# Kernel tuning notes

Hardware: AMD Instinct MI355X
Metric: run time of the kernel (lower is better)

Reference implementation:

```python
import jax, jax.numpy as jnp
import numpy as np

NOT_EPSILON = 1.0
B, K, Q, T = 2, 512, 512, 128


def swishmax(x, axis):
    # x * exp(x - max) normalized by sum(|.|) + 1 along `axis`
    xexp = x * jnp.exp(x - jnp.max(x, axis=axis, keepdims=True))
    return xexp / (jnp.sum(jnp.abs(xexp), axis=axis, keepdims=True) + NOT_EPSILON)


def setup_inputs() -> dict:
    key = jax.random.key(0)
    ks = jax.random.split(key, 8)
    scale = 1.0 / np.sqrt(T)
    return {
        "query_tokens": jax.random.normal(ks[0], (B, Q, T), dtype=jnp.float32),
        "key_tokens": jax.random.normal(ks[1], (B, K, T), dtype=jnp.float32),
        "value_tokens": jax.random.normal(ks[2], (B, K, T), dtype=jnp.float32),
        "Wk": jax.random.normal(ks[3], (T, T), dtype=jnp.float32) * scale,
        "Wq": jax.random.normal(ks[4], (T, T), dtype=jnp.float32) * scale,
        "Wv": jax.random.normal(ks[5], (T, T), dtype=jnp.float32) * scale,
        "Wl": jax.random.normal(ks[6], (T, T), dtype=jnp.float32) * scale,
        "Wo": jax.random.normal(ks[7], (T, T), dtype=jnp.float32) * scale,
    }


def reference(query_tokens, key_tokens, value_tokens, Wk, Wq, Wv, Wl, Wo):
    lin = lambda x, W: jnp.einsum('...t,ut->...u', x, W)  # nn.Linear(bias=False): x @ W.T
    k = lin(key_tokens, Wk)       # [B, K, T]
    q = lin(query_tokens, Wq)     # [B, Q, T]
    # outer-product broadcast over tokens: [B, K, Q, T]
    attention_raw = k[..., :, None, :] * q[..., None, :, :]
    attention_logits = lin(attention_raw, Wl)            # [B, K, Q, T]
    attention_scale = swishmax(attention_logits, axis=-2)  # normalize over Q (dim=-2)
    v = lin(value_tokens, Wv)     # [B, K, T]
    values_scaled = v[..., :, None, :] * attention_scale  # [B, K, Q, T]
    value_sum = values_scaled.sum(axis=-3)                # sum over K -> [B, Q, T]
    return lin(value_sum, Wo)
```

## Files before the change

### kernel.cpp

```cpp
#include <hip/hip_runtime.h>


using f16    = _Float16;
using f16x4  = __attribute__((ext_vector_type(4)))  f16;
using f16x8  = __attribute__((ext_vector_type(8)))  f16;
using f32x16 = __attribute__((ext_vector_type(16))) float;

#define LOG2E 1.4426950408889634f

__device__ __forceinline__ float exp2b(float x) {
  return __builtin_amdgcn_exp2f(x);
}

__device__ __forceinline__ f16x8 cvt8(float4 a, float4 b) {
  f16x8 r;
  r[0]=(f16)a.x; r[1]=(f16)a.y; r[2]=(f16)a.z; r[3]=(f16)a.w;
  r[4]=(f16)b.x; r[5]=(f16)b.y; r[6]=(f16)b.z; r[7]=(f16)b.w;
  return r;
}

__global__ __launch_bounds__(256, 2) void k1_proj(
    const float* __restrict__ q_tok, const float* __restrict__ k_tok,
    const float* __restrict__ v_tok, const float* __restrict__ Wq,
    const float* __restrict__ Wk,    const float* __restrict__ Wv,
    f16* __restrict__ qh, float* __restrict__ kls, float* __restrict__ vf)
{
  const int gid    = blockIdx.x;
  const int tensor = gid >> 4;
  const int sub    = gid & 15;
  const int b      = sub >> 3;
  const int rt     = sub & 7;
  const float* X = tensor==0 ? q_tok : (tensor==1 ? k_tok : v_tok);
  const float* W = tensor==0 ? Wq    : (tensor==1 ? Wk    : Wv);

  const int tid = threadIdx.x;
  const int w = tid >> 6, lane = tid & 63;
  const int l31 = lane & 31, lhi = lane >> 5;
  const int rbase = rt*64 + (w>>1)*32;
  const int cbase = (w&1)*64;

  f32x16 C0, C1;
  #pragma unroll
  for (int i=0;i<16;++i){ C0[i]=0.f; C1[i]=0.f; }

  #pragma unroll
  for (int kc=0; kc<8; ++kc) {
    const float* ap = X + (size_t)(b*512 + rbase + l31)*128 + kc*16 + 8*lhi;
    f16x8 a = cvt8(*(const float4*)ap, *(const float4*)(ap+4));
    const float* bp0 = W + (size_t)(cbase + l31)*128 + kc*16 + 8*lhi;
    f16x8 b0 = cvt8(*(const float4*)bp0, *(const float4*)(bp0+4));
    C0 = __builtin_amdgcn_mfma_f32_32x32x16_f16(a, b0, C0, 0, 0, 0);
    const float* bp1 = bp0 + 32*128;
    f16x8 b1 = cvt8(*(const float4*)bp1, *(const float4*)(bp1+4));
    C1 = __builtin_amdgcn_mfma_f32_32x32x16_f16(a, b1, C1, 0, 0, 0);
  }

  #pragma unroll
  for (int us=0; us<2; ++us) {
    #pragma unroll
    for (int r=0; r<16; ++r) {
      const int row = rbase + (r&3) + 8*(r>>2) + 4*lhi;
      const int col = cbase + us*32 + l31;
      const float val = us ? C1[r] : C0[r];
      const size_t idx = (size_t)(b*512 + row)*128 + col;
      if (tensor==0)      qh[idx]  = (f16)val;
      else if (tensor==1) kls[idx] = val * LOG2E;
      else                vf[idx]  = val;
    }
  }
}

__global__ __launch_bounds__(1024, 4) void k2_main(
    const f16* __restrict__ qh, const float* __restrict__ kls,
    const float* __restrict__ vf, const float* __restrict__ Wl,
    f16* __restrict__ part)
{
  const int gid  = blockIdx.x;
  const int b    = gid >> 7;
  const int uq   = (gid >> 5) & 3;
  const int grp  = gid & 31;
  const int kk0  = grp * 16;

  const int tid = threadIdx.x;
  const int w = tid >> 6, lane = tid & 63;
  const int l31 = lane & 31, lhi = lane >> 5;
  const int ubase = uq * 32;
  const int qbase = w * 32;

  __shared__ f16    Bl[2][2][32][136];
  __shared__ float4 red[2][16][32];

  f16x8 af[8];
  {
    const f16* ab = qh + (size_t)(b*512 + qbase + l31)*128 + 8*lhi;
    #pragma unroll
    for (int kc=0; kc<8; ++kc) af[kc] = *(const f16x8*)(ab + kc*16);
  }

  const int bu = tid >> 5;
  const int tc = tid & 31;
  const float4 wl = *(const float4*)(Wl + (size_t)(ubase + bu)*128 + tc*4);

  const float* kbase = kls + (size_t)(b*512 + kk0)*128 + tc*4;
  const float* vbase = vf  + (size_t)(b*512 + kk0)*128 + ubase;

  f32x16 acc;
  #pragma unroll
  for (int i=0;i<16;++i) acc[i]=0.f;

  {
    const float4 ka = *(const float4*)(kbase);
    const float4 kb = *(const float4*)(kbase + 128);
    f16x4 oa, ob;
    oa[0]=(f16)(wl.x*ka.x); oa[1]=(f16)(wl.y*ka.y);
    oa[2]=(f16)(wl.z*ka.z); oa[3]=(f16)(wl.w*ka.w);
    ob[0]=(f16)(wl.x*kb.x); ob[1]=(f16)(wl.y*kb.y);
    ob[2]=(f16)(wl.z*kb.z); ob[3]=(f16)(wl.w*kb.w);
    *(f16x4*)(&Bl[0][0][bu][tc*4]) = oa;
    *(f16x4*)(&Bl[0][1][bu][tc*4]) = ob;
  }
  float4 na = *(const float4*)(kbase + 256);
  float4 nb = *(const float4*)(kbase + 384);
  __syncthreads();

  for (int i=0; i<8; ++i) {
    const int cur = i & 1;

    const float v0 = vbase[(2*i)*128   + l31];
    const float v1 = vbase[(2*i+1)*128 + l31];

    if (i < 7) {
      f16x4 oa, ob;
      oa[0]=(f16)(wl.x*na.x); oa[1]=(f16)(wl.y*na.y);
      oa[2]=(f16)(wl.z*na.z); oa[3]=(f16)(wl.w*na.w);
      ob[0]=(f16)(wl.x*nb.x); ob[1]=(f16)(wl.y*nb.y);
      ob[2]=(f16)(wl.z*nb.z); ob[3]=(f16)(wl.w*nb.w);
      *(f16x4*)(&Bl[cur^1][0][bu][tc*4]) = oa;
      *(f16x4*)(&Bl[cur^1][1][bu][tc*4]) = ob;
      if (i < 6) {
        na = *(const float4*)(kbase + (2*i+4)*128);
        nb = *(const float4*)(kbase + (2*i+5)*128);
      }
    }

    f32x16 C0, C1;
    #pragma unroll
    for (int j=0;j<16;++j){ C0[j]=0.f; C1[j]=0.f; }
    __builtin_amdgcn_s_setprio(1);
    #pragma unroll
    for (int kc=0; kc<8; ++kc) {
      f16x8 b0 = *(const f16x8*)(&Bl[cur][0][l31][kc*16 + 8*lhi]);
      f16x8 b1 = *(const f16x8*)(&Bl[cur][1][l31][kc*16 + 8*lhi]);
      C0 = __builtin_amdgcn_mfma_f32_32x32x16_f16(af[kc], b0, C0, 0,0,0);
      C1 = __builtin_amdgcn_mfma_f32_32x32x16_f16(af[kc], b1, C1, 0,0,0);
    }
    __builtin_amdgcn_s_setprio(0);

    float mx0a=-3.4e38f, mx0b=-3.4e38f, s0a=0.f, s0b=0.f;
    float mx1a=-3.4e38f, mx1b=-3.4e38f, s1a=0.f, s1b=0.f;
    #pragma unroll
    for (int r=0; r<16; ++r) {
      const float y0 = C0[r], y1 = C1[r];
      const float p0 = y0 * exp2b(y0);
      const float p1 = y1 * exp2b(y1);
      C0[r] = p0; C1[r] = p1;
      if (r & 1) { mx0b=fmaxf(mx0b,y0); s0b+=fabsf(p0);
                   mx1b=fmaxf(mx1b,y1); s1b+=fabsf(p1); }
      else       { mx0a=fmaxf(mx0a,y0); s0a+=fabsf(p0);
                   mx1a=fmaxf(mx1a,y1); s1a+=fabsf(p1); }
    }
    float mx0 = fmaxf(mx0a,mx0b), mx1 = fmaxf(mx1a,mx1b);
    float sm0 = s0a+s0b,          sm1 = s1a+s1b;
    mx0 = fmaxf(mx0, __shfl_xor(mx0, 32));
    mx1 = fmaxf(mx1, __shfl_xor(mx1, 32));
    sm0 += __shfl_xor(sm0, 32);
    sm1 += __shfl_xor(sm1, 32);
    if (lane < 32)
      red[cur][w][lane] = make_float4(mx0, sm0, mx1, sm1);

    __syncthreads();

    float M0=-3.4e38f, S0=0.f, M1=-3.4e38f, S1=0.f;
    #pragma unroll
    for (int j=0; j<8; ++j) {
      const float4 t = red[cur][8*lhi + j][l31];
      M0 = fmaxf(M0, t.x); S0 += t.y;
      M1 = fmaxf(M1, t.z); S1 += t.w;
    }
    M0 = fmaxf(M0, __shfl_xor(M0, 32));
    S0 += __shfl_xor(S0, 32);
    M1 = fmaxf(M1, __shfl_xor(M1, 32));
    S1 += __shfl_xor(S1, 32);

    const float su0 = v0 / (S0 + LOG2E * exp2b(M0));
    const float su1 = v1 / (S1 + LOG2E * exp2b(M1));

    #pragma unroll
    for (int r=0; r<16; ++r) {
      acc[r] = fmaf(su0, C0[r], acc[r]);
      acc[r] = fmaf(su1, C1[r], acc[r]);
    }
  }

  {
    const int s = (grp<<3) + (b<<2) + uq;
    f16* pbase = part + (size_t)s*16384 + l31;
    #pragma unroll
    for (int r=0; r<16; ++r) {
      const int q = qbase + (r&3) + 8*(r>>2) + 4*lhi;
      pbase[q*32] = (f16)acc[r];
    }
  }
}

__global__ __launch_bounds__(256, 2) void k3_out(
    const f16* __restrict__ part, const float* __restrict__ Wo,
    float* __restrict__ out)
{
  const int gid = blockIdx.x;
  const int qt = gid >> 1, b = gid & 1;
  const int rbase = qt * 32;
  const int tid = threadIdx.x;

  __shared__ f16 vt[32][136];

  {
    const int q  = tid >> 3;
    const int uc = tid & 7;
    const int uq  = uc >> 1;
    const int ul0 = (uc & 1) * 16;

    float s[16];
    #pragma unroll
    for (int j=0;j<16;++j) s[j]=0.f;

    const f16* pb = part + (size_t)((b<<2) + uq)*16384 + (rbase + q)*32 + ul0;
    for (int g=0; g<32; ++g) {
      const f16x8 p0 = *(const f16x8*)(pb + (size_t)g*131072);
      const f16x8 p1 = *(const f16x8*)(pb + (size_t)g*131072 + 8);
      #pragma unroll
      for (int j=0;j<8;++j) { s[j] += (float)p0[j]; s[8+j] += (float)p1[j]; }
    }
    f16x8 o0, o1;
    #pragma unroll
    for (int j=0;j<8;++j) { o0[j] = (f16)s[j]; o1[j] = (f16)s[8+j]; }
    *(f16x8*)(&vt[q][uc*16])     = o0;
    *(f16x8*)(&vt[q][uc*16 + 8]) = o1;
  }
  __syncthreads();

  const int w = tid >> 6, lane = tid & 63;
  const int l31 = lane & 31, lhi = lane >> 5;
  const int cbase = w * 32;

  f32x16 C;
  #pragma unroll
  for (int i=0;i<16;++i) C[i] = 0.f;

  #pragma unroll
  for (int kc=0; kc<8; ++kc) {
    f16x8 a = *(const f16x8*)(&vt[l31][kc*16 + 8*lhi]);
    const float* bp = Wo + (size_t)(cbase + l31)*128 + kc*16 + 8*lhi;
    f16x8 bfr = cvt8(*(const float4*)bp, *(const float4*)(bp+4));
    C = __builtin_amdgcn_mfma_f32_32x32x16_f16(a, bfr, C, 0, 0, 0);
  }

  #pragma unroll
  for (int r=0; r<16; ++r) {
    const int row = rbase + (r&3) + 8*(r>>2) + 4*lhi;
    const int col = cbase + l31;
    out[(size_t)(b*512 + row)*128 + col] = C[r];
  }
}

extern "C" void kernel_launch(void* const* d_in, const int* in_sizes, int n_in,
                              void* d_out, int out_size, void* d_ws, size_t ws_size,
                              hipStream_t stream) {
  const float* q_tok = (const float*)d_in[0];
  const float* k_tok = (const float*)d_in[1];
  const float* v_tok = (const float*)d_in[2];
  const float* Wk    = (const float*)d_in[3];
  const float* Wq    = (const float*)d_in[4];
  const float* Wv    = (const float*)d_in[5];
  const float* Wl    = (const float*)d_in[6];
  const float* Wo    = (const float*)d_in[7];

  char* ws = (char*)d_ws;
  f16*   qh   = (f16*)  (ws);
  float* kls  = (float*)(ws + 262144);
  float* vf   = (float*)(ws + 786432);
  f16*   part = (f16*)  (ws + 1310720);

  k1_proj<<<48, 256, 0, stream>>>(q_tok, k_tok, v_tok, Wq, Wk, Wv, qh, kls, vf);
  k2_main<<<256, 1024, 0, stream>>>(qh, kls, vf, Wl, part);
  k3_out<<<32, 256, 0, stream>>>(part, Wo, (float*)d_out);
}
```

Before: 116.7 us.

## Give each k2 wave 64 query rows and halve the block size

Each wave of the main kernel now computes two 32-row query tiles against the same LDS B fragments. Blocks shrink from 1024 to 512 threads, and the cross-wave swishmax reduction covers 8 waves instead of 16. The Wl*k staging is rewritten so each thread converts 8 elements per row with wider loads and stores. This reuses LDS reads across more MFMAs and cuts barrier participants, at the cost of roughly double accumulator and A-fragment register pressure, which may lower occupancy.

```diff
diff --git a/kernel.cpp b/kernel.cpp
--- a/kernel.cpp
+++ b/kernel.cpp
@@ -2,7 +2,6 @@
 
 
 using f16    = _Float16;
-using f16x4  = __attribute__((ext_vector_type(4)))  f16;
 using f16x8  = __attribute__((ext_vector_type(8)))  f16;
 using f32x16 = __attribute__((ext_vector_type(16))) float;
 
@@ -70,7 +69,7 @@
   }
 }
 
-__global__ __launch_bounds__(1024, 4) void k2_main(
+__global__ __launch_bounds__(512, 2) void k2_main(
     const f16* __restrict__ qh, const float* __restrict__ kls,
     const float* __restrict__ vf, const float* __restrict__ Wl,
     f16* __restrict__ part)
@@ -85,42 +84,50 @@
   const int w = tid >> 6, lane = tid & 63;
   const int l31 = lane & 31, lhi = lane >> 5;
   const int ubase = uq * 32;
-  const int qbase = w * 32;
+  const int qbase = w * 64;
 
   __shared__ f16    Bl[2][2][32][136];
-  __shared__ float4 red[2][16][32];
-
-  f16x8 af[8];
+  __shared__ float4 red[2][8][32];
+
+  f16x8 af[2][8];
   {
     const f16* ab = qh + (size_t)(b*512 + qbase + l31)*128 + 8*lhi;
     #pragma unroll
-    for (int kc=0; kc<8; ++kc) af[kc] = *(const f16x8*)(ab + kc*16);
-  }
-
-  const int bu = tid >> 5;
-  const int tc = tid & 31;
-  const float4 wl = *(const float4*)(Wl + (size_t)(ubase + bu)*128 + tc*4);
-
-  const float* kbase = kls + (size_t)(b*512 + kk0)*128 + tc*4;
+    for (int qs=0; qs<2; ++qs)
+      #pragma unroll
+      for (int kc=0; kc<8; ++kc)
+        af[qs][kc] = *(const f16x8*)(ab + qs*32*128 + kc*16);
+  }
+
+  const int bu  = tid >> 4;
+  const int btc = tid & 15;
+  const float* wlr = Wl + (size_t)(ubase + bu)*128 + btc*8;
+  const float4 wl0 = *(const float4*)(wlr);
+  const float4 wl1 = *(const float4*)(wlr+4);
+
+  const float* kbase = kls + (size_t)(b*512 + kk0)*128 + btc*8;
   const float* vbase = vf  + (size_t)(b*512 + kk0)*128 + ubase;
 
-  f32x16 acc;
-  #pragma unroll
-  for (int i=0;i<16;++i) acc[i]=0.f;
+  f32x16 acc[2];
+  #pragma unroll
+  for (int i=0;i<16;++i){ acc[0][i]=0.f; acc[1][i]=0.f; }
 
   {
-    const float4 ka = *(const float4*)(kbase);
-    const float4 kb = *(const float4*)(kbase + 128);
-    f16x4 oa, ob;
-    oa[0]=(f16)(wl.x*ka.x); oa[1]=(f16)(wl.y*ka.y);
-    oa[2]=(f16)(wl.z*ka.z); oa[3]=(f16)(wl.w*ka.w);
-    ob[0]=(f16)(wl.x*kb.x); ob[1]=(f16)(wl.y*kb.y);
-    ob[2]=(f16)(wl.z*kb.z); ob[3]=(f16)(wl.w*kb.w);
-    *(f16x4*)(&Bl[0][0][bu][tc*4]) = oa;
-    *(f16x4*)(&Bl[0][1][bu][tc*4]) = ob;
-  }
-  float4 na = *(const float4*)(kbase + 256);
-  float4 nb = *(const float4*)(kbase + 384);
+    const float4 ka0 = *(const float4*)(kbase);
+    const float4 ka1 = *(const float4*)(kbase+4);
+    const float4 kb0 = *(const float4*)(kbase+128);
+    const float4 kb1 = *(const float4*)(kbase+132);
+    float4 a0 = make_float4(wl0.x*ka0.x, wl0.y*ka0.y, wl0.z*ka0.z, wl0.w*ka0.w);
+    float4 a1 = make_float4(wl1.x*ka1.x, wl1.y*ka1.y, wl1.z*ka1.z, wl1.w*ka1.w);
+    float4 b0 = make_float4(wl0.x*kb0.x, wl0.y*kb0.y, wl0.z*kb0.z, wl0.w*kb0.w);
+    float4 b1 = make_float4(wl1.x*kb1.x, wl1.y*kb1.y, wl1.z*kb1.z, wl1.w*kb1.w);
+    *(f16x8*)(&Bl[0][0][bu][btc*8]) = cvt8(a0, a1);
+    *(f16x8*)(&Bl[0][1][bu][btc*8]) = cvt8(b0, b1);
+  }
+  float4 na0 = *(const float4*)(kbase+256);
+  float4 na1 = *(const float4*)(kbase+260);
+  float4 nb0 = *(const float4*)(kbase+384);
+  float4 nb1 = *(const float4*)(kbase+388);
   __syncthreads();
 
   for (int i=0; i<8; ++i) {
@@ -130,29 +137,31 @@
     const float v1 = vbase[(2*i+1)*128 + l31];
 
     if (i < 7) {
-      f16x4 oa, ob;
-      oa[0]=(f16)(wl.x*na.x); oa[1]=(f16)(wl.y*na.y);
-      oa[2]=(f16)(wl.z*na.z); oa[3]=(f16)(wl.w*na.w);
-      ob[0]=(f16)(wl.x*nb.x); ob[1]=(f16)(wl.y*nb.y);
-      ob[2]=(f16)(wl.z*nb.z); ob[3]=(f16)(wl.w*nb.w);
-      *(f16x4*)(&Bl[cur^1][0][bu][tc*4]) = oa;
-      *(f16x4*)(&Bl[cur^1][1][bu][tc*4]) = ob;
+      float4 a0 = make_float4(wl0.x*na0.x, wl0.y*na0.y, wl0.z*na0.z, wl0.w*na0.w);
+      float4 a1 = make_float4(wl1.x*na1.x, wl1.y*na1.y, wl1.z*na1.z, wl1.w*na1.w);
+      float4 b0 = make_float4(wl0.x*nb0.x, wl0.y*nb0.y, wl0.z*nb0.z, wl0.w*nb0.w);
+      float4 b1 = make_float4(wl1.x*nb1.x, wl1.y*nb1.y, wl1.z*nb1.z, wl1.w*nb1.w);
+      *(f16x8*)(&Bl[cur^1][0][bu][btc*8]) = cvt8(a0, a1);
+      *(f16x8*)(&Bl[cur^1][1][bu][btc*8]) = cvt8(b0, b1);
       if (i < 6) {
-        na = *(const float4*)(kbase + (2*i+4)*128);
-        nb = *(const float4*)(kbase + (2*i+5)*128);
+        const float* kp = kbase + (2*i+4)*128;
+        na0 = *(const float4*)(kp);     na1 = *(const float4*)(kp+4);
+        nb0 = *(const float4*)(kp+128); nb1 = *(const float4*)(kp+132);
       }
     }
 
-    f32x16 C0, C1;
-    #pragma unroll
-    for (int j=0;j<16;++j){ C0[j]=0.f; C1[j]=0.f; }
+    f32x16 C00, C01, C10, C11;
+    #pragma unroll
+    for (int j=0;j<16;++j){ C00[j]=0.f; C01[j]=0.f; C10[j]=0.f; C11[j]=0.f; }
     __builtin_amdgcn_s_setprio(1);
     #pragma unroll
     for (int kc=0; kc<8; ++kc) {
       f16x8 b0 = *(const f16x8*)(&Bl[cur][0][l31][kc*16 + 8*lhi]);
       f16x8 b1 = *(const f16x8*)(&Bl[cur][1][l31][kc*16 + 8*lhi]);
-      C0 = __builtin_amdgcn_mfma_f32_32x32x16_f16(af[kc], b0, C0, 0,0,0);
-      C1 = __builtin_amdgcn_mfma_f32_32x32x16_f16(af[kc], b1, C1, 0,0,0);
+      C00 = __builtin_amdgcn_mfma_f32_32x32x16_f16(af[0][kc], b0, C00, 0,0,0);
+      C10 = __builtin_amdgcn_mfma_f32_32x32x16_f16(af[1][kc], b0, C10, 0,0,0);
+      C01 = __builtin_amdgcn_mfma_f32_32x32x16_f16(af[0][kc], b1, C01, 0,0,0);
+      C11 = __builtin_amdgcn_mfma_f32_32x32x16_f16(af[1][kc], b1, C11, 0,0,0);
     }
     __builtin_amdgcn_s_setprio(0);
 
@@ -160,14 +169,17 @@
     float mx1a=-3.4e38f, mx1b=-3.4e38f, s1a=0.f, s1b=0.f;
     #pragma unroll
     for (int r=0; r<16; ++r) {
-      const float y0 = C0[r], y1 = C1[r];
-      const float p0 = y0 * exp2b(y0);
-      const float p1 = y1 * exp2b(y1);
-      C0[r] = p0; C1[r] = p1;
-      if (r & 1) { mx0b=fmaxf(mx0b,y0); s0b+=fabsf(p0);
-                   mx1b=fmaxf(mx1b,y1); s1b+=fabsf(p1); }
-      else       { mx0a=fmaxf(mx0a,y0); s0a+=fabsf(p0);
-                   mx1a=fmaxf(mx1a,y1); s1a+=fabsf(p1); }
+      const float y00 = C00[r], y01 = C01[r];
+      const float y10 = C10[r], y11 = C11[r];
+      const float p00 = y00 * exp2b(y00);
+      const float p01 = y01 * exp2b(y01);
+      const float p10 = y10 * exp2b(y10);
+      const float p11 = y11 * exp2b(y11);
+      C00[r] = p00; C01[r] = p01; C10[r] = p10; C11[r] = p11;
+      if (r & 1) { mx0b=fmaxf(mx0b,fmaxf(y00,y10)); s0b+=fabsf(p00)+fabsf(p10);
+                   mx1b=fmaxf(mx1b,fmaxf(y01,y11)); s1b+=fabsf(p01)+fabsf(p11); }
+      else       { mx0a=fmaxf(mx0a,fmaxf(y00,y10)); s0a+=fabsf(p00)+fabsf(p10);
+                   mx1a=fmaxf(mx1a,fmaxf(y01,y11)); s1a+=fabsf(p01)+fabsf(p11); }
     }
     float mx0 = fmaxf(mx0a,mx0b), mx1 = fmaxf(mx1a,mx1b);
     float sm0 = s0a+s0b,          sm1 = s1a+s1b;
@@ -182,8 +194,8 @@
 
     float M0=-3.4e38f, S0=0.f, M1=-3.4e38f, S1=0.f;
     #pragma unroll
-    for (int j=0; j<8; ++j) {
-      const float4 t = red[cur][8*lhi + j][l31];
+    for (int j=0; j<4; ++j) {
+      const float4 t = red[cur][4*lhi + j][l31];
       M0 = fmaxf(M0, t.x); S0 += t.y;
       M1 = fmaxf(M1, t.z); S1 += t.w;
     }
@@ -197,8 +209,10 @@
 
     #pragma unroll
     for (int r=0; r<16; ++r) {
-      acc[r] = fmaf(su0, C0[r], acc[r]);
-      acc[r] = fmaf(su1, C1[r], acc[r]);
+      acc[0][r] = fmaf(su0, C00[r], acc[0][r]);
+      acc[0][r] = fmaf(su1, C01[r], acc[0][r]);
+      acc[1][r] = fmaf(su0, C10[r], acc[1][r]);
+      acc[1][r] = fmaf(su1, C11[r], acc[1][r]);
     }
   }
 
@@ -206,10 +220,12 @@
     const int s = (grp<<3) + (b<<2) + uq;
     f16* pbase = part + (size_t)s*16384 + l31;
     #pragma unroll
-    for (int r=0; r<16; ++r) {
-      const int q = qbase + (r&3) + 8*(r>>2) + 4*lhi;
-      pbase[q*32] = (f16)acc[r];
-    }
+    for (int qs=0; qs<2; ++qs)
+      #pragma unroll
+      for (int r=0; r<16; ++r) {
+        const int q = qbase + qs*32 + (r&3) + 8*(r>>2) + 4*lhi;
+        pbase[q*32] = (f16)acc[qs][r];
+      }
   }
 }
 
@@ -292,6 +308,6 @@
   f16*   part = (f16*)  (ws + 1310720);
 
   k1_proj<<<48, 256, 0, stream>>>(q_tok, k_tok, v_tok, Wq, Wk, Wv, qh, kls, vf);
-  k2_main<<<256, 1024, 0, stream>>>(qh, kls, vf, Wl, part);
+  k2_main<<<256, 512, 0, stream>>>(qh, kls, vf, Wl, part);
   k3_out<<<32, 256, 0, stream>>>(part, Wo, (float*)d_out);
 }
```

Measured after the change: 114.2 us. 1.02x faster.
